# Optimization experiments

Hardware: AMD Instinct MI355X
Metric: run time of the kernel (lower is better)

Reference implementation:

```python
import jax, jax.numpy as jnp
import numpy as np

B, L, CTX, PRED = 128, 96, 96, 24
S, STEPS, HID = 100, 16, 256
IN_DIM = PRED + 2 + CTX  # z + t + h + scaled context


def setup_inputs() -> dict:
    key = jax.random.key(0)
    ks = jax.random.split(key, 6)
    sc = lambda k, sh, fan: (jax.random.normal(k, sh, jnp.float32) / np.sqrt(fan)).astype(jnp.float32)
    return {
        "past_target": jax.random.normal(ks[0], (B, L), jnp.float32),
        "past_observed_values": jnp.ones((B, L), jnp.float32),
        "z0": jax.random.normal(ks[1], (S, B, PRED), jnp.float32),  # pre-drawn noise, one per sample
        "W1": sc(ks[2], (IN_DIM, HID), IN_DIM), "b1": jnp.zeros((HID,), jnp.float32),
        "W2": sc(ks[3], (HID, HID), HID), "b2": jnp.zeros((HID,), jnp.float32),
        "W3": sc(ks[4], (HID, PRED), HID), "b3": jnp.zeros((PRED,), jnp.float32),
    }


def _net(z, t, ctx, W1, b1, W2, b2, W3, b3):
    # z: (S,B,P), t: scalar, ctx: (B,CTX) -> velocity (S,B,P)
    Sn, Bn = z.shape[0], z.shape[1]
    tfeat = jnp.full((Sn, Bn, 1), t, z.dtype)
    hfeat = jnp.zeros((Sn, Bn, 1), z.dtype)
    cfeat = jnp.broadcast_to(ctx[None], (Sn, Bn, ctx.shape[-1]))
    x = jnp.concatenate([z, tfeat, hfeat, cfeat], axis=-1)  # (S,B,IN_DIM)
    h = jax.nn.relu(x @ W1 + b1)
    h = jax.nn.relu(h @ W2 + b2)
    return h @ W3 + b3


def reference(past_target, past_observed_values, z0, W1, b1, W2, b2, W3, b3):
    ctx = past_target[:, -CTX:]                                     # (B,CTX)
    loc = jnp.clip(jnp.mean(jnp.abs(ctx), axis=1, keepdims=True), 1e-6, None)  # (B,1)
    scaled_ctx = ctx / loc
    dt = 1.0 / STEPS
    t_vals = 1.0 - jnp.arange(STEPS, dtype=jnp.float32) * dt        # t = 1, 1-dt, ...

    def step(z, t):
        v = _net(z, t, scaled_ctx, W1, b1, W2, b2, W3, b3)
        return z - dt * v, None

    zT, _ = jax.lax.scan(step, z0, t_vals)                          # (S,B,P)
    preds = zT * loc[None]                                          # unscale
    return jnp.transpose(preds, (1, 0, 2))                          # (B,S,P) == torch.stack(dim=1)
```

## Files before the change

### kernel.cpp

```cpp
#include <hip/hip_runtime.h>

#define NB 128
#define NS 100
#define NPRED 24
#define NHID 256
#define NSTEPS 16
#define NCTX 96

typedef float f32x4 __attribute__((ext_vector_type(4)));
typedef short bf16x8 __attribute__((ext_vector_type(8)));

__device__ __forceinline__ unsigned short f2bf(float f) {
    union { float f; unsigned u; } v; v.f = f;
    return (unsigned short)((v.u + 0x7fffu + ((v.u >> 16) & 1u)) >> 16);
}
__device__ __forceinline__ unsigned cvtpk(float lo, float hi) {
    unsigned r;
    asm("v_cvt_pk_bf16_f32 %0, %1, %2" : "=v"(r) : "v"(lo), "v"(hi));
    return r;
}
__device__ __forceinline__ bf16x8 mk8(unsigned a, unsigned b, unsigned c, unsigned d) {
    union { unsigned u[4]; bf16x8 v; } x;
    x.u[0] = a; x.u[1] = b; x.u[2] = c; x.u[3] = d;
    return x.v;
}
__device__ __forceinline__ f32x4 bf4_to_f32x4(const unsigned short* pA) {
    uint2 uu = *(const uint2*)pA;
    union { unsigned u; float f; } c0, c1, c2, c3;
    c0.u = uu.x << 16; c1.u = uu.x & 0xffff0000u;
    c2.u = uu.y << 16; c3.u = uu.y & 0xffff0000u;
    f32x4 r; r.x = c0.f; r.y = c1.f; r.z = c2.f; r.w = c3.f;
    return r;
}
__device__ __forceinline__ f32x4 relu4(f32x4 a) {
    a.x = fmaxf(a.x, 0.f); a.y = fmaxf(a.y, 0.f);
    a.z = fmaxf(a.z, 0.f); a.w = fmaxf(a.w, 0.f);
    return a;
}


__global__ void prep_kernel(const float* __restrict__ past_target,
                            const float* __restrict__ W1,
                            const float* __restrict__ b1,
                            const float* __restrict__ W2,
                            const float* __restrict__ W3,
                            unsigned short* __restrict__ wsf) {
    int blk = blockIdx.x;
    if (blk < NB) {
        int b = blk, j = threadIdx.x;
        const float* ctxp = past_target + b * NCTX;
        float asum = 0.f;
        for (int k = 0; k < NCTX; k++) asum += fabsf(ctxp[k]);
        float loc = fmaxf(asum * (1.f / (float)NCTX), 1e-6f);
        float inv = 1.f / loc;
        if (j == 0) ((float*)(wsf + 114688))[b] = loc;
        float acc = b1[j];
        for (int k = 0; k < NCTX; k++)
            acc += (ctxp[k] * inv) * W1[(26 + k) * NHID + j];
        wsf[81920 + b * NHID + j] = f2bf(acc);
        return;
    }
    int i = (blk - NB) * 256 + threadIdx.x;
    if (i < 8192) {
        int T = i >> 9, ll = (i >> 3) & 63, e = i & 7;
        int k = 16 * (e >> 2) + 4 * (ll >> 4) + (e & 3);
        int m = 16 * T + (ll & 15);
        wsf[i] = (k <= 24) ? f2bf(W1[k * NHID + m]) : (unsigned short)0;
    } else if (i < 16384) {
        int idx = i - 8192;
        int ks = idx >> 10, T = (idx >> 9) & 1, ll = (idx >> 3) & 63, e = idx & 7;
        int k = 32 * ks + 16 * (e >> 2) + 4 * (ll >> 4) + (e & 3);
        int m = 16 * T + (ll & 15);
        wsf[i] = (m < NPRED) ? f2bf(W3[k * NPRED + m]) : (unsigned short)0;
    } else {
        int idx = i - 16384;
        int ks = idx >> 13, T = (idx >> 9) & 15, ll = (idx >> 3) & 63, e = idx & 7;
        int k = 32 * ks + 16 * (e >> 2) + 4 * (ll >> 4) + (e & 3);
        int m = 16 * T + (ll & 15);
        wsf[i] = f2bf(W2[k * NHID + m]);
    }
}

__global__ __launch_bounds__(256, 2) void fm_kernel(
    const float* __restrict__ z0g,
    const float* __restrict__ b2, const float* __restrict__ b3,
    const unsigned short* __restrict__ wsf,
    float* __restrict__ out) {
    __shared__ __attribute__((aligned(16))) unsigned exA[2048];
    __shared__ __attribute__((aligned(16))) float vredV[2048];

    const int tid = threadIdx.x;
    const int g = blockIdx.x;

    const int w = tid >> 6;
    const int l = tid & 63;
    const int q = l >> 4, p = l & 15;
    const int R = g * 16 + p;
    const int s = R >> 7, b = R & 127;
    const int l8 = l * 8;
    const int l4 = l * 4;

    bf16x8 w1r[4];
    bf16x8 w2r[32];
    bf16x8 w3r[4];
#pragma unroll
    for (int j = 0; j < 4; j++)
        w1r[j] = *(const bf16x8*)(wsf + (4 * w + j) * 512 + l8);
#pragma unroll
    for (int ks = 0; ks < 8; ks++)
#pragma unroll
        for (int j = 0; j < 4; j++)
            w2r[ks * 4 + j] = *(const bf16x8*)(wsf + 16384 + (ks * 16 + 4 * w + j) * 512 + l8);
#pragma unroll
    for (int d = 0; d < 2; d++)
#pragma unroll
        for (int tt = 0; tt < 2; tt++)
            w3r[2 * d + tt] = *(const bf16x8*)(wsf + 8192 + (2 * w + d) * 1024 + tt * 512 + l8);

    f32x4 cbr[4];
#pragma unroll
    for (int j = 0; j < 4; j++)
        cbr[j] = bf4_to_f32x4(wsf + 81920 + b * NHID + (4 * w + j) * 16 + 4 * q);

    f32x4 b2f[4];
#pragma unroll
    for (int j = 0; j < 4; j++)
        b2f[j] = *(const f32x4*)(b2 + (4 * w + j) * 16 + 4 * q);
    f32x4 b3f0 = *(const f32x4*)(b3 + 4 * q);
    f32x4 b3f1 = {0.f, 0.f, 0.f, 0.f};
    if (q < 2) b3f1 = *(const f32x4*)(b3 + 16 + 4 * q);

    f32x4 zs0, zs1;
    {
        const f32x4* zr = (const f32x4*)(z0g + R * NPRED);
        zs0 = zr[q];
        f32x4 zz = {0.f, 0.f, 0.f, 0.f};
        zs1 = zz;
        if (q < 2) zs1 = zr[4 + q];
    }

    const float dt = 1.f / (float)NSTEPS;
#pragma unroll 1
    for (int step = 0; step < NSTEPS; step++) {
        float t = 1.f - (float)step * dt;
        float z10 = (q == 2) ? t : zs1.x;
        bf16x8 bz = mk8(cvtpk(zs0.x, zs0.y), cvtpk(zs0.z, zs0.w),
                        cvtpk(z10, zs1.y), cvtpk(zs1.z, zs1.w));

        {
            f32x4 h0 = relu4(__builtin_amdgcn_mfma_f32_16x16x32_bf16(w1r[0], bz, cbr[0], 0, 0, 0));
            f32x4 h1 = relu4(__builtin_amdgcn_mfma_f32_16x16x32_bf16(w1r[1], bz, cbr[1], 0, 0, 0));
            uint4 t0;
            t0.x = cvtpk(h0.x, h0.y); t0.y = cvtpk(h0.z, h0.w);
            t0.z = cvtpk(h1.x, h1.y); t0.w = cvtpk(h1.z, h1.w);
            *(uint4*)(exA + (2 * w) * 256 + l4) = t0;
            f32x4 h2 = relu4(__builtin_amdgcn_mfma_f32_16x16x32_bf16(w1r[2], bz, cbr[2], 0, 0, 0));
            f32x4 h3 = relu4(__builtin_amdgcn_mfma_f32_16x16x32_bf16(w1r[3], bz, cbr[3], 0, 0, 0));
            uint4 t1;
            t1.x = cvtpk(h2.x, h2.y); t1.y = cvtpk(h2.z, h2.w);
            t1.z = cvtpk(h3.x, h3.y); t1.w = cvtpk(h3.z, h3.w);
            *(uint4*)(exA + (2 * w + 1) * 256 + l4) = t1;
        }
        __syncthreads();

        f32x4 a0 = {0.f, 0.f, 0.f, 0.f}, a1 = a0, a2 = a0, a3 = a0;
#pragma unroll
        for (int ks = 0; ks < 8; ks++) {
            uint4 bw = *(const uint4*)(exA + ks * 256 + l4);
            bf16x8 bb = mk8(bw.x, bw.y, bw.z, bw.w);
            a0 = __builtin_amdgcn_mfma_f32_16x16x32_bf16(w2r[ks * 4 + 0], bb, a0, 0, 0, 0);
            a1 = __builtin_amdgcn_mfma_f32_16x16x32_bf16(w2r[ks * 4 + 1], bb, a1, 0, 0, 0);
            a2 = __builtin_amdgcn_mfma_f32_16x16x32_bf16(w2r[ks * 4 + 2], bb, a2, 0, 0, 0);
            a3 = __builtin_amdgcn_mfma_f32_16x16x32_bf16(w2r[ks * 4 + 3], bb, a3, 0, 0, 0);
        }
        unsigned bh2[8];
        {
            f32x4 h0 = relu4(a0 + b2f[0]), h1 = relu4(a1 + b2f[1]);
            f32x4 h2 = relu4(a2 + b2f[2]), h3 = relu4(a3 + b2f[3]);
            bh2[0] = cvtpk(h0.x, h0.y); bh2[1] = cvtpk(h0.z, h0.w);
            bh2[2] = cvtpk(h1.x, h1.y); bh2[3] = cvtpk(h1.z, h1.w);
            bh2[4] = cvtpk(h2.x, h2.y); bh2[5] = cvtpk(h2.z, h2.w);
            bh2[6] = cvtpk(h3.x, h3.y); bh2[7] = cvtpk(h3.z, h3.w);
        }

        f32x4 v0 = {0.f, 0.f, 0.f, 0.f}, v1 = v0;
        {
            bf16x8 bbA = mk8(bh2[0], bh2[1], bh2[2], bh2[3]);
            bf16x8 bbB = mk8(bh2[4], bh2[5], bh2[6], bh2[7]);
            v0 = __builtin_amdgcn_mfma_f32_16x16x32_bf16(w3r[0], bbA, v0, 0, 0, 0);
            v1 = __builtin_amdgcn_mfma_f32_16x16x32_bf16(w3r[1], bbA, v1, 0, 0, 0);
            v0 = __builtin_amdgcn_mfma_f32_16x16x32_bf16(w3r[2], bbB, v0, 0, 0, 0);
            v1 = __builtin_amdgcn_mfma_f32_16x16x32_bf16(w3r[3], bbB, v1, 0, 0, 0);
        }
        *(f32x4*)(vredV + (2 * w) * 256 + l4) = v0;
        *(f32x4*)(vredV + (2 * w + 1) * 256 + l4) = v1;
        __syncthreads();

        f32x4 sv0 = {0.f, 0.f, 0.f, 0.f}, sv1 = sv0;
#pragma unroll
        for (int w2 = 0; w2 < 4; w2++) {
            f32x4 t0 = *(const f32x4*)(vredV + (2 * w2) * 256 + l4);
            f32x4 t1 = *(const f32x4*)(vredV + (2 * w2 + 1) * 256 + l4);
            sv0.x += t0.x; sv0.y += t0.y; sv0.z += t0.z; sv0.w += t0.w;
            sv1.x += t1.x; sv1.y += t1.y; sv1.z += t1.z; sv1.w += t1.w;
        }

        zs0.x -= dt * (sv0.x + b3f0.x); zs0.y -= dt * (sv0.y + b3f0.y);
        zs0.z -= dt * (sv0.z + b3f0.z); zs0.w -= dt * (sv0.w + b3f0.w);
        zs1.x -= dt * (sv1.x + b3f1.x); zs1.y -= dt * (sv1.y + b3f1.y);
        zs1.z -= dt * (sv1.z + b3f1.z); zs1.w -= dt * (sv1.w + b3f1.w);
    }

    if (w == 0) {
        float loc = ((const float*)(wsf + 114688))[b];
        float* op = out + b * (NS * NPRED) + s * NPRED;
        f32x4 o0 = zs0 * loc;
        *(f32x4*)(op + 4 * q) = o0;
        if (q < 2) { f32x4 o1 = zs1 * loc; *(f32x4*)(op + 16 + 4 * q) = o1; }
    }
}

extern "C" void kernel_launch(void* const* d_in, const int* in_sizes, int n_in,
                              void* d_out, int out_size, void* d_ws, size_t ws_size,
                              hipStream_t stream) {
    const float* past_target = (const float*)d_in[0];
    const float* z0 = (const float*)d_in[2];
    const float* W1 = (const float*)d_in[3];
    const float* b1 = (const float*)d_in[4];
    const float* W2 = (const float*)d_in[5];
    const float* b2 = (const float*)d_in[6];
    const float* W3 = (const float*)d_in[7];
    const float* b3 = (const float*)d_in[8];

    unsigned short* wsf = (unsigned short*)d_ws;

    prep_kernel<<<448, 256, 0, stream>>>(past_target, W1, b1, W2, W3, wsf);
    fm_kernel<<<800, 256, 0, stream>>>(z0, b2, b3, wsf, (float*)d_out);
}
```

Before: 49.71 us.

## Split hidden dimension across eight waves per block to cut per-thread registers

Doubles the block to 512 threads so each wave owns 32 hidden channels instead of 64, halving the per-wave W1/W2 register tiles and MFMA count per step. W3 fragments are now reloaded from global memory each step instead of staying in registers, and the b2 and dt*b3 biases are packed as bf16 to save registers. The cross-wave velocity reduction grows from four to eight partials in shared memory. The goals are higher occupancy and shorter per-step critical paths, at the cost of larger reductions, per-step W3 loads, and bf16 rounding of the biases.

```diff
diff --git a/kernel.cpp b/kernel.cpp
--- a/kernel.cpp
+++ b/kernel.cpp
@@ -29,6 +29,13 @@
     union { unsigned u; float f; } c0, c1, c2, c3;
     c0.u = uu.x << 16; c1.u = uu.x & 0xffff0000u;
     c2.u = uu.y << 16; c3.u = uu.y & 0xffff0000u;
+    f32x4 r; r.x = c0.f; r.y = c1.f; r.z = c2.f; r.w = c3.f;
+    return r;
+}
+__device__ __forceinline__ f32x4 up4(unsigned a, unsigned b) {
+    union { unsigned u; float f; } c0, c1, c2, c3;
+    c0.u = a << 16; c1.u = a & 0xffff0000u;
+    c2.u = b << 16; c3.u = b & 0xffff0000u;
     f32x4 r; r.x = c0.f; r.y = c1.f; r.z = c2.f; r.w = c3.f;
     return r;
 }
@@ -81,13 +88,13 @@
     }
 }
 
-__global__ __launch_bounds__(256, 2) void fm_kernel(
+__global__ __launch_bounds__(512, 4) void fm_kernel(
     const float* __restrict__ z0g,
     const float* __restrict__ b2, const float* __restrict__ b3,
     const unsigned short* __restrict__ wsf,
     float* __restrict__ out) {
     __shared__ __attribute__((aligned(16))) unsigned exA[2048];
-    __shared__ __attribute__((aligned(16))) float vredV[2048];
+    __shared__ __attribute__((aligned(16))) float vredV[4096];
 
     const int tid = threadIdx.x;
     const int g = blockIdx.x;
@@ -100,35 +107,39 @@
     const int l8 = l * 8;
     const int l4 = l * 4;
 
-    bf16x8 w1r[4];
-    bf16x8 w2r[32];
-    bf16x8 w3r[4];
-#pragma unroll
-    for (int j = 0; j < 4; j++)
-        w1r[j] = *(const bf16x8*)(wsf + (4 * w + j) * 512 + l8);
+    bf16x8 w1r[2];
+    bf16x8 w2r[16];
+#pragma unroll
+    for (int tt = 0; tt < 2; tt++)
+        w1r[tt] = *(const bf16x8*)(wsf + (2 * w + tt) * 512 + l8);
 #pragma unroll
     for (int ks = 0; ks < 8; ks++)
 #pragma unroll
-        for (int j = 0; j < 4; j++)
-            w2r[ks * 4 + j] = *(const bf16x8*)(wsf + 16384 + (ks * 16 + 4 * w + j) * 512 + l8);
-#pragma unroll
-    for (int d = 0; d < 2; d++)
-#pragma unroll
         for (int tt = 0; tt < 2; tt++)
-            w3r[2 * d + tt] = *(const bf16x8*)(wsf + 8192 + (2 * w + d) * 1024 + tt * 512 + l8);
-
-    f32x4 cbr[4];
-#pragma unroll
-    for (int j = 0; j < 4; j++)
-        cbr[j] = bf4_to_f32x4(wsf + 81920 + b * NHID + (4 * w + j) * 16 + 4 * q);
-
-    f32x4 b2f[4];
-#pragma unroll
-    for (int j = 0; j < 4; j++)
-        b2f[j] = *(const f32x4*)(b2 + (4 * w + j) * 16 + 4 * q);
-    f32x4 b3f0 = *(const f32x4*)(b3 + 4 * q);
-    f32x4 b3f1 = {0.f, 0.f, 0.f, 0.f};
-    if (q < 2) b3f1 = *(const f32x4*)(b3 + 16 + 4 * q);
+            w2r[2 * ks + tt] = *(const bf16x8*)(wsf + 16384 + (ks * 16 + 2 * w + tt) * 512 + l8);
+
+    f32x4 cbr[2];
+#pragma unroll
+    for (int tt = 0; tt < 2; tt++)
+        cbr[tt] = bf4_to_f32x4(wsf + 81920 + b * NHID + (2 * w + tt) * 16 + 4 * q);
+
+    unsigned b2p[4];
+#pragma unroll
+    for (int tt = 0; tt < 2; tt++) {
+        int ch = (2 * w + tt) * 16 + 4 * q;
+        b2p[2 * tt]     = cvtpk(b2[ch], b2[ch + 1]);
+        b2p[2 * tt + 1] = cvtpk(b2[ch + 2], b2[ch + 3]);
+    }
+    const float dt = 1.f / (float)NSTEPS;
+    unsigned dtb3p[4];
+    {
+        f32x4 b3f0 = *(const f32x4*)(b3 + 4 * q);
+        f32x4 b3f1 = {0.f, 0.f, 0.f, 0.f};
+        if (q < 2) b3f1 = *(const f32x4*)(b3 + 16 + 4 * q);
+        f32x4 d0 = b3f0 * dt, d1 = b3f1 * dt;
+        dtb3p[0] = cvtpk(d0.x, d0.y); dtb3p[1] = cvtpk(d0.z, d0.w);
+        dtb3p[2] = cvtpk(d1.x, d1.y); dtb3p[3] = cvtpk(d1.z, d1.w);
+    }
 
     f32x4 zs0, zs1;
     {
@@ -139,9 +150,13 @@
         if (q < 2) zs1 = zr[4 + q];
     }
 
-    const float dt = 1.f / (float)NSTEPS;
 #pragma unroll 1
     for (int step = 0; step < NSTEPS; step++) {
+        const unsigned short* w3p = wsf + 8192 + w * 1024 + l8;
+        asm volatile("" : "+v"(w3p));
+        bf16x8 w3f0 = *(const bf16x8*)(w3p);
+        bf16x8 w3f1 = *(const bf16x8*)(w3p + 512);
+
         float t = 1.f - (float)step * dt;
         float z10 = (q == 2) ? t : zs1.x;
         bf16x8 bz = mk8(cvtpk(zs0.x, zs0.y), cvtpk(zs0.z, zs0.w),
@@ -153,44 +168,31 @@
             uint4 t0;
             t0.x = cvtpk(h0.x, h0.y); t0.y = cvtpk(h0.z, h0.w);
             t0.z = cvtpk(h1.x, h1.y); t0.w = cvtpk(h1.z, h1.w);
-            *(uint4*)(exA + (2 * w) * 256 + l4) = t0;
-            f32x4 h2 = relu4(__builtin_amdgcn_mfma_f32_16x16x32_bf16(w1r[2], bz, cbr[2], 0, 0, 0));
-            f32x4 h3 = relu4(__builtin_amdgcn_mfma_f32_16x16x32_bf16(w1r[3], bz, cbr[3], 0, 0, 0));
-            uint4 t1;
-            t1.x = cvtpk(h2.x, h2.y); t1.y = cvtpk(h2.z, h2.w);
-            t1.z = cvtpk(h3.x, h3.y); t1.w = cvtpk(h3.z, h3.w);
-            *(uint4*)(exA + (2 * w + 1) * 256 + l4) = t1;
+            *(uint4*)(exA + w * 256 + l4) = t0;
         }
         __syncthreads();
 
-        f32x4 a0 = {0.f, 0.f, 0.f, 0.f}, a1 = a0, a2 = a0, a3 = a0;
+        f32x4 a0 = {0.f, 0.f, 0.f, 0.f}, a1 = a0;
 #pragma unroll
         for (int ks = 0; ks < 8; ks++) {
             uint4 bw = *(const uint4*)(exA + ks * 256 + l4);
             bf16x8 bb = mk8(bw.x, bw.y, bw.z, bw.w);
-            a0 = __builtin_amdgcn_mfma_f32_16x16x32_bf16(w2r[ks * 4 + 0], bb, a0, 0, 0, 0);
-            a1 = __builtin_amdgcn_mfma_f32_16x16x32_bf16(w2r[ks * 4 + 1], bb, a1, 0, 0, 0);
-            a2 = __builtin_amdgcn_mfma_f32_16x16x32_bf16(w2r[ks * 4 + 2], bb, a2, 0, 0, 0);
-            a3 = __builtin_amdgcn_mfma_f32_16x16x32_bf16(w2r[ks * 4 + 3], bb, a3, 0, 0, 0);
-        }
-        unsigned bh2[8];
-        {
-            f32x4 h0 = relu4(a0 + b2f[0]), h1 = relu4(a1 + b2f[1]);
-            f32x4 h2 = relu4(a2 + b2f[2]), h3 = relu4(a3 + b2f[3]);
+            a0 = __builtin_amdgcn_mfma_f32_16x16x32_bf16(w2r[2 * ks], bb, a0, 0, 0, 0);
+            a1 = __builtin_amdgcn_mfma_f32_16x16x32_bf16(w2r[2 * ks + 1], bb, a1, 0, 0, 0);
+        }
+        unsigned bh2[4];
+        {
+            f32x4 h0 = relu4(a0 + up4(b2p[0], b2p[1]));
+            f32x4 h1 = relu4(a1 + up4(b2p[2], b2p[3]));
             bh2[0] = cvtpk(h0.x, h0.y); bh2[1] = cvtpk(h0.z, h0.w);
             bh2[2] = cvtpk(h1.x, h1.y); bh2[3] = cvtpk(h1.z, h1.w);
-            bh2[4] = cvtpk(h2.x, h2.y); bh2[5] = cvtpk(h2.z, h2.w);
-            bh2[6] = cvtpk(h3.x, h3.y); bh2[7] = cvtpk(h3.z, h3.w);
         }
 
         f32x4 v0 = {0.f, 0.f, 0.f, 0.f}, v1 = v0;
         {
             bf16x8 bbA = mk8(bh2[0], bh2[1], bh2[2], bh2[3]);
-            bf16x8 bbB = mk8(bh2[4], bh2[5], bh2[6], bh2[7]);
-            v0 = __builtin_amdgcn_mfma_f32_16x16x32_bf16(w3r[0], bbA, v0, 0, 0, 0);
-            v1 = __builtin_amdgcn_mfma_f32_16x16x32_bf16(w3r[1], bbA, v1, 0, 0, 0);
-            v0 = __builtin_amdgcn_mfma_f32_16x16x32_bf16(w3r[2], bbB, v0, 0, 0, 0);
-            v1 = __builtin_amdgcn_mfma_f32_16x16x32_bf16(w3r[3], bbB, v1, 0, 0, 0);
+            v0 = __builtin_amdgcn_mfma_f32_16x16x32_bf16(w3f0, bbA, v0, 0, 0, 0);
+            v1 = __builtin_amdgcn_mfma_f32_16x16x32_bf16(w3f1, bbA, v1, 0, 0, 0);
         }
         *(f32x4*)(vredV + (2 * w) * 256 + l4) = v0;
         *(f32x4*)(vredV + (2 * w + 1) * 256 + l4) = v1;
@@ -198,17 +200,20 @@
 
         f32x4 sv0 = {0.f, 0.f, 0.f, 0.f}, sv1 = sv0;
 #pragma unroll
-        for (int w2 = 0; w2 < 4; w2++) {
+        for (int w2 = 0; w2 < 8; w2++) {
             f32x4 t0 = *(const f32x4*)(vredV + (2 * w2) * 256 + l4);
             f32x4 t1 = *(const f32x4*)(vredV + (2 * w2 + 1) * 256 + l4);
             sv0.x += t0.x; sv0.y += t0.y; sv0.z += t0.z; sv0.w += t0.w;
             sv1.x += t1.x; sv1.y += t1.y; sv1.z += t1.z; sv1.w += t1.w;
         }
 
-        zs0.x -= dt * (sv0.x + b3f0.x); zs0.y -= dt * (sv0.y + b3f0.y);
-        zs0.z -= dt * (sv0.z + b3f0.z); zs0.w -= dt * (sv0.w + b3f0.w);
-        zs1.x -= dt * (sv1.x + b3f1.x); zs1.y -= dt * (sv1.y + b3f1.y);
-        zs1.z -= dt * (sv1.z + b3f1.z); zs1.w -= dt * (sv1.w + b3f1.w);
+        {
+            f32x4 d0 = up4(dtb3p[0], dtb3p[1]), d1 = up4(dtb3p[2], dtb3p[3]);
+            zs0.x -= dt * sv0.x + d0.x; zs0.y -= dt * sv0.y + d0.y;
+            zs0.z -= dt * sv0.z + d0.z; zs0.w -= dt * sv0.w + d0.w;
+            zs1.x -= dt * sv1.x + d1.x; zs1.y -= dt * sv1.y + d1.y;
+            zs1.z -= dt * sv1.z + d1.z; zs1.w -= dt * sv1.w + d1.w;
+        }
     }
 
     if (w == 0) {
@@ -235,5 +240,5 @@
     unsigned short* wsf = (unsigned short*)d_ws;
 
     prep_kernel<<<448, 256, 0, stream>>>(past_target, W1, b1, W2, W3, wsf);
-    fm_kernel<<<800, 256, 0, stream>>>(z0, b2, b3, wsf, (float*)d_out);
-}
+    fm_kernel<<<800, 512, 0, stream>>>(z0, b2, b3, wsf, (float*)d_out);
+}
```

Result: slower. 78.93 us (+58.8%).

## Compute full layer-1 redundantly per wave from LDS to drop a barrier

Applied to the files above, without the earlier changes.

Each wave now computes all 16 tiles of the first layer itself, reading W1 and the context-bias term from shared memory staged once at kernel start. This removes the per-step LDS exchange of layer-1 activations and its __syncthreads. The velocity reduction buffer is double-buffered by step parity, so the remaining barrier per step is enough without a WAR hazard. The cost is 4x redundant layer-1 MFMAs, extra LDS reads each step, and more registers for the bh array, which may pressure occupancy at launch_bounds(256,2).

```diff
diff --git a/kernel.cpp b/kernel.cpp
--- a/kernel.cpp
+++ b/kernel.cpp
@@ -86,11 +86,24 @@
     const float* __restrict__ b2, const float* __restrict__ b3,
     const unsigned short* __restrict__ wsf,
     float* __restrict__ out) {
-    __shared__ __attribute__((aligned(16))) unsigned exA[2048];
-    __shared__ __attribute__((aligned(16))) float vredV[2048];
+    __shared__ __attribute__((aligned(16))) unsigned short W1L[8192];
+    __shared__ __attribute__((aligned(16))) unsigned short cbL[4096];
+    __shared__ __attribute__((aligned(16))) float vredD[2][2048];
 
     const int tid = threadIdx.x;
     const int g = blockIdx.x;
+
+    {
+        const uint4* src = (const uint4*)wsf;
+        uint4* dst = (uint4*)W1L;
+        for (int i = tid; i < 1024; i += 256) dst[i] = src[i];
+        for (int idx = tid; idx < 4096; idx += 256) {
+            int T = idx >> 8, r2 = idx & 255, qq = r2 >> 6, p4 = r2 & 63;
+            int p = p4 >> 2, ii = p4 & 3;
+            int bb = (g * 16 + p) & 127;
+            cbL[idx] = wsf[81920 + bb * NHID + 16 * T + 4 * qq + ii];
+        }
+    }
 
     const int w = tid >> 6;
     const int l = tid & 63;
@@ -100,13 +113,9 @@
     const int l8 = l * 8;
     const int l4 = l * 4;
 
-    bf16x8 w1r[4];
     bf16x8 w2r[32];
     bf16x8 w3r[4];
 #pragma unroll
-    for (int j = 0; j < 4; j++)
-        w1r[j] = *(const bf16x8*)(wsf + (4 * w + j) * 512 + l8);
-#pragma unroll
     for (int ks = 0; ks < 8; ks++)
 #pragma unroll
         for (int j = 0; j < 4; j++)
@@ -116,11 +125,6 @@
 #pragma unroll
         for (int tt = 0; tt < 2; tt++)
             w3r[2 * d + tt] = *(const bf16x8*)(wsf + 8192 + (2 * w + d) * 1024 + tt * 512 + l8);
-
-    f32x4 cbr[4];
-#pragma unroll
-    for (int j = 0; j < 4; j++)
-        cbr[j] = bf4_to_f32x4(wsf + 81920 + b * NHID + (4 * w + j) * 16 + 4 * q);
 
     f32x4 b2f[4];
 #pragma unroll
@@ -139,35 +143,31 @@
         if (q < 2) zs1 = zr[4 + q];
     }
 
+    __syncthreads();
+
     const float dt = 1.f / (float)NSTEPS;
 #pragma unroll 1
     for (int step = 0; step < NSTEPS; step++) {
+        float* vred = &vredD[step & 1][0];
         float t = 1.f - (float)step * dt;
         float z10 = (q == 2) ? t : zs1.x;
         bf16x8 bz = mk8(cvtpk(zs0.x, zs0.y), cvtpk(zs0.z, zs0.w),
                         cvtpk(z10, zs1.y), cvtpk(zs1.z, zs1.w));
 
-        {
-            f32x4 h0 = relu4(__builtin_amdgcn_mfma_f32_16x16x32_bf16(w1r[0], bz, cbr[0], 0, 0, 0));
-            f32x4 h1 = relu4(__builtin_amdgcn_mfma_f32_16x16x32_bf16(w1r[1], bz, cbr[1], 0, 0, 0));
-            uint4 t0;
-            t0.x = cvtpk(h0.x, h0.y); t0.y = cvtpk(h0.z, h0.w);
-            t0.z = cvtpk(h1.x, h1.y); t0.w = cvtpk(h1.z, h1.w);
-            *(uint4*)(exA + (2 * w) * 256 + l4) = t0;
-            f32x4 h2 = relu4(__builtin_amdgcn_mfma_f32_16x16x32_bf16(w1r[2], bz, cbr[2], 0, 0, 0));
-            f32x4 h3 = relu4(__builtin_amdgcn_mfma_f32_16x16x32_bf16(w1r[3], bz, cbr[3], 0, 0, 0));
-            uint4 t1;
-            t1.x = cvtpk(h2.x, h2.y); t1.y = cvtpk(h2.z, h2.w);
-            t1.z = cvtpk(h3.x, h3.y); t1.w = cvtpk(h3.z, h3.w);
-            *(uint4*)(exA + (2 * w + 1) * 256 + l4) = t1;
-        }
-        __syncthreads();
+        unsigned bh[32];
+#pragma unroll
+        for (int T = 0; T < 16; T++) {
+            bf16x8 a = *(const bf16x8*)(W1L + T * 512 + l8);
+            f32x4 c = bf4_to_f32x4(cbL + T * 256 + q * 64 + p * 4);
+            f32x4 h = relu4(__builtin_amdgcn_mfma_f32_16x16x32_bf16(a, bz, c, 0, 0, 0));
+            bh[2 * T]     = cvtpk(h.x, h.y);
+            bh[2 * T + 1] = cvtpk(h.z, h.w);
+        }
 
         f32x4 a0 = {0.f, 0.f, 0.f, 0.f}, a1 = a0, a2 = a0, a3 = a0;
 #pragma unroll
         for (int ks = 0; ks < 8; ks++) {
-            uint4 bw = *(const uint4*)(exA + ks * 256 + l4);
-            bf16x8 bb = mk8(bw.x, bw.y, bw.z, bw.w);
+            bf16x8 bb = mk8(bh[4 * ks], bh[4 * ks + 1], bh[4 * ks + 2], bh[4 * ks + 3]);
             a0 = __builtin_amdgcn_mfma_f32_16x16x32_bf16(w2r[ks * 4 + 0], bb, a0, 0, 0, 0);
             a1 = __builtin_amdgcn_mfma_f32_16x16x32_bf16(w2r[ks * 4 + 1], bb, a1, 0, 0, 0);
             a2 = __builtin_amdgcn_mfma_f32_16x16x32_bf16(w2r[ks * 4 + 2], bb, a2, 0, 0, 0);
@@ -192,15 +192,15 @@
             v0 = __builtin_amdgcn_mfma_f32_16x16x32_bf16(w3r[2], bbB, v0, 0, 0, 0);
             v1 = __builtin_amdgcn_mfma_f32_16x16x32_bf16(w3r[3], bbB, v1, 0, 0, 0);
         }
-        *(f32x4*)(vredV + (2 * w) * 256 + l4) = v0;
-        *(f32x4*)(vredV + (2 * w + 1) * 256 + l4) = v1;
+        *(f32x4*)(vred + (2 * w) * 256 + l4) = v0;
+        *(f32x4*)(vred + (2 * w + 1) * 256 + l4) = v1;
         __syncthreads();
 
         f32x4 sv0 = {0.f, 0.f, 0.f, 0.f}, sv1 = sv0;
 #pragma unroll
         for (int w2 = 0; w2 < 4; w2++) {
-            f32x4 t0 = *(const f32x4*)(vredV + (2 * w2) * 256 + l4);
-            f32x4 t1 = *(const f32x4*)(vredV + (2 * w2 + 1) * 256 + l4);
+            f32x4 t0 = *(const f32x4*)(vred + (2 * w2) * 256 + l4);
+            f32x4 t1 = *(const f32x4*)(vred + (2 * w2 + 1) * 256 + l4);
             sv0.x += t0.x; sv0.y += t0.y; sv0.z += t0.z; sv0.w += t0.w;
             sv1.x += t1.x; sv1.y += t1.y; sv1.z += t1.z; sv1.w += t1.w;
         }
```

After: 87.57 us. +76.1%, slower.
